# Optimization experiments

Measured on AMD Instinct MI355X. Metric: run time of the kernel, lower is better.

## Reference

```python
import jax, jax.numpy as jnp
import numpy as np

N = 100000   # total nodes
E = 600000   # total edges
G = 2048     # graphs in batch
DIN = 9      # input node feature dim
D = 128      # hidden == output dim
L = 5        # GIN layers
BN_EPS = 1e-5
LN_EPS = 1e-5


def setup_inputs() -> dict:
    key = jax.random.key(0)
    ks = jax.random.split(key, 24)
    s = 0.05
    x = jax.random.normal(ks[0], (N, DIN), jnp.float32)
    edge_index = jax.random.randint(ks[1], (2, E), 0, N, dtype=jnp.int32)
    batch = jnp.sort(jax.random.randint(ks[2], (N,), 0, G, dtype=jnp.int32))
    return {
        "x": x,
        "edge_index": edge_index,
        "batch": batch,
        # node embedding
        "node_emb_W": jax.random.normal(ks[3], (DIN, D), jnp.float32) * s,
        "node_emb_b": jnp.zeros((D,), jnp.float32),
        # GIN layer MLPs, stacked over layers: Linear(D,2D) -> ReLU -> Linear(2D,D)
        "W1s": jax.random.normal(ks[4], (L, D, 2 * D), jnp.float32) * s,
        "b1s": jnp.zeros((L, 2 * D), jnp.float32),
        "W2s": jax.random.normal(ks[5], (L, 2 * D, D), jnp.float32) * s,
        "b2s": jnp.zeros((L, D), jnp.float32),
        # BatchNorm affine params per layer
        "bn_g": jnp.ones((L, D), jnp.float32),
        "bn_b": jnp.zeros((L, D), jnp.float32),
        # virtual node
        "vn_emb": jax.random.normal(ks[6], (1, D), jnp.float32),
        "vn_W1": jax.random.normal(ks[7], (D, D), jnp.float32) * s,
        "vn_b1": jnp.zeros((D,), jnp.float32),
        "vn_W2": jax.random.normal(ks[8], (D, D), jnp.float32) * s,
        "vn_b2": jnp.zeros((D,), jnp.float32),
        # graph MLP: Linear -> LayerNorm -> ReLU -> Linear
        "gm_W1": jax.random.normal(ks[9], (D, D), jnp.float32) * s,
        "gm_b1": jnp.zeros((D,), jnp.float32),
        "ln_g": jnp.ones((D,), jnp.float32),
        "ln_b": jnp.zeros((D,), jnp.float32),
        "gm_W2": jax.random.normal(ks[10], (D, D), jnp.float32) * s,
        "gm_b2": jnp.zeros((D,), jnp.float32),
    }


def _mean_pool(h, batch):
    # segment mean over graphs: [N, D] -> [G, D]
    s = jax.ops.segment_sum(h, batch, num_segments=G)
    cnt = jax.ops.segment_sum(jnp.ones((h.shape[0], 1), h.dtype), batch, num_segments=G)
    return s / jnp.maximum(cnt, 1.0)


def _batchnorm(m, g, b):
    mu = jnp.mean(m, axis=0)
    var = jnp.mean(jnp.square(m - mu), axis=0)  # biased var (torch train-mode norm)
    return (m - mu) * jax.lax.rsqrt(var + BN_EPS) * g + b


def reference(x, edge_index, batch, node_emb_W, node_emb_b, W1s, b1s, W2s, b2s,
              bn_g, bn_b, vn_emb, vn_W1, vn_b1, vn_W2, vn_b2,
              gm_W1, gm_b1, ln_g, ln_b, gm_W2, gm_b2):
    src, dst = edge_index[0], edge_index[1]
    h = x @ node_emb_W + node_emb_b                       # [N, D]
    vn = jnp.tile(vn_emb, (G, 1))                         # [G, D]
    for i in range(L):
        h_prev = h
        # GINConv (eps=0): mlp(h + sum_{j->i} h_j) via gather/scatter-add
        agg = jax.ops.segment_sum(h[src], dst, num_segments=N)
        m = h + agg
        m = jax.nn.relu(m @ W1s[i] + b1s[i]) @ W2s[i] + b2s[i]
        h = jax.nn.relu(_batchnorm(m, bn_g[i], bn_b[i]))
        # (dropout is identity in eval mode)
        if i > 0:
            h = h + h_prev
        # virtual node: pool -> MLP -> broadcast back
        temp = _mean_pool(h, batch)                       # [G, D]
        vn = vn + (jax.nn.relu(temp @ vn_W1 + vn_b1) @ vn_W2 + vn_b2)
        h = h + vn[batch]
    node_features = h                                     # output_projection = Identity
    gf = _mean_pool(node_features, batch)                 # [G, D]
    gf = gf @ gm_W1 + gm_b1
    mu = jnp.mean(gf, axis=-1, keepdims=True)
    var = jnp.mean(jnp.square(gf - mu), axis=-1, keepdims=True)
    gf = (gf - mu) * jax.lax.rsqrt(var + LN_EPS) * ln_g + ln_b
    gf = jax.nn.relu(gf)
    graph_features = gf @ gm_W2 + gm_b2
    return node_features, graph_features
```

## Files before the change

kernel.cpp:

```cpp
#include <hip/hip_runtime.h>
#include <stdint.h>

#define NNODES 100000
#define NEDGES 600000
#define NGRAPH 2048
#define DD 128
#define NLAYER 5
#define NPAD 100096
#define SCAN_NB 391
#define NSTAT 32

typedef __attribute__((ext_vector_type(8))) __bf16 bf16x8;
typedef __attribute__((ext_vector_type(4))) float f32x4;
typedef __attribute__((ext_vector_type(8))) ushort u16x8;

__device__ __forceinline__ ushort f2b(float f) {
    union { float f; uint32_t u; } v; v.f = f;
    uint32_t r = v.u + 0x7FFFu + ((v.u >> 16) & 1u);
    return (ushort)(r >> 16);
}

__device__ __forceinline__ float b2f(ushort u) {
    union { uint32_t u; float f; } v; v.u = ((uint32_t)u) << 16; return v.f;
}

__device__ __forceinline__ void gload_lds16(const void* g, void* l) {
    __builtin_amdgcn_global_load_lds(
        (const __attribute__((address_space(1))) void*)g,
        (__attribute__((address_space(3))) void*)l, 16, 0, 0);
}

__global__ void prep_w_kernel(const float* __restrict__ W1s, const float* __restrict__ W2s,
                              ushort* __restrict__ w1t, ushort* __restrict__ w2t) {
    int idx = blockIdx.x * 256 + threadIdx.x;
    const int per = 128 * 256;
    if (idx < NLAYER * per) {
        int i = idx / per, rem = idx % per;
        int n = rem >> 7, k = rem & 127;
        w1t[idx] = f2b(W1s[(size_t)i * per + k * 256 + n]);
    } else if (idx < 2 * NLAYER * per) {
        int j = idx - NLAYER * per;
        int i = j / per, rem = j % per;
        int n = rem >> 8, k = rem & 255;
        w2t[j] = f2b(W2s[(size_t)i * per + k * 128 + n]);
    }
}

__global__ void node_embed_kernel(const float* __restrict__ x, const float* __restrict__ W,
                                  const float* __restrict__ b, ushort* __restrict__ hb,
                                  const float* __restrict__ vne, float* __restrict__ vn) {
    int idx = blockIdx.x * 256 + threadIdx.x;
    if (idx < NNODES * 128) {
        int n = idx >> 7, d = idx & 127;
        float v = b[d];
#pragma unroll
        for (int k = 0; k < 9; ++k) v += x[n * 9 + k] * W[k * 128 + d];
        hb[(size_t)n * 128 + d] = f2b(v);
    } else if (idx < NNODES * 128 + NGRAPH * 128) {
        int r = idx - NNODES * 128;
        vn[r] = vne[r & 127];
    }
}


__global__ void deg_kernel(const int* __restrict__ dst, int* __restrict__ deg) {
    int e = blockIdx.x * 256 + threadIdx.x;
    if (e < NEDGES) atomicAdd(&deg[dst[e]], 1);
}

__global__ void scan_part_kernel(const int* __restrict__ deg, int* __restrict__ partials) {
    int i = blockIdx.x * 256 + threadIdx.x;
    int lane = threadIdx.x & 63, w = threadIdx.x >> 6;
    int v = (i < NNODES) ? deg[i] : 0;
#pragma unroll
    for (int o = 1; o < 64; o <<= 1) v += __shfl_xor(v, o);
    __shared__ int ws[4];
    if (lane == 0) ws[w] = v;
    __syncthreads();
    if (threadIdx.x == 0) partials[blockIdx.x] = ws[0] + ws[1] + ws[2] + ws[3];
}

__global__ __launch_bounds__(512)
void scan_top_kernel(int* __restrict__ partials) {
    __shared__ int s[512];
    int t = threadIdx.x;
    int v = (t < SCAN_NB) ? partials[t] : 0;
    s[t] = v;
    __syncthreads();
#pragma unroll
    for (int o = 1; o < 512; o <<= 1) {
        int n = (t >= o) ? s[t - o] : 0;
        __syncthreads();
        s[t] += n;
        __syncthreads();
    }
    if (t < SCAN_NB) partials[t] = s[t] - v;
}

__global__ void scan_blocks_kernel(const int* __restrict__ deg, const int* __restrict__ partials,
                                   int* __restrict__ rs, int* __restrict__ cursor) {
    int i = blockIdx.x * 256 + threadIdx.x;
    int lane = threadIdx.x & 63, w = threadIdx.x >> 6;
    int v = (i < NNODES) ? deg[i] : 0;
    int x = v;
#pragma unroll
    for (int o = 1; o < 64; o <<= 1) {
        int n = __shfl_up(x, o);
        if (lane >= o) x += n;
    }
    __shared__ int ws[4];
    if (lane == 63) ws[w] = x;
    __syncthreads();
    if (threadIdx.x == 0) {
        int a = 0;
#pragma unroll
        for (int k = 0; k < 4; ++k) { int t = ws[k]; ws[k] = a; a += t; }
    }
    __syncthreads();
    int excl = (x - v) + ws[w] + partials[blockIdx.x];
    if (i < NNODES) { rs[i] = excl; cursor[i] = excl; }
    if (i == 0) rs[NNODES] = NEDGES;
}

__global__ void csr_scatter_kernel(const int* __restrict__ src, const int* __restrict__ dst,
                                   int* __restrict__ cursor, int* __restrict__ csrc) {
    int e = blockIdx.x * 256 + threadIdx.x;
    if (e < NEDGES) {
        int p = atomicAdd(&cursor[dst[e]], 1);
        csrc[p] = src[e];
    }
}

__device__ __forceinline__ int lbound(const int* __restrict__ b, int key) {
    int lo = 0, hi = NNODES;
    while (lo < hi) { int m = (lo + hi) >> 1; if (b[m] < key) lo = m + 1; else hi = m; }
    return lo;
}

__global__ void gstart_kernel(const int* __restrict__ batch, int* __restrict__ gstart,
                              float* __restrict__ inv) {
    int g = blockIdx.x * 256 + threadIdx.x;
    if (g <= NGRAPH)
        gstart[g] = (g == NGRAPH) ? NNODES : lbound(batch, g);
    if (g < NGRAPH) {
        int c = lbound(batch, g + 1) - lbound(batch, g);
        inv[g] = 1.f / (float)(c > 0 ? c : 1);
    }
}


__global__ __launch_bounds__(256)
void gin_agg_kernel(const ushort* __restrict__ hb, const int* __restrict__ rs,
                    const int* __restrict__ csrc, ushort* __restrict__ xb,
                    float* __restrict__ stats) {
    if (blockIdx.x < NSTAT) stats[blockIdx.x * 256 + threadIdx.x] = 0.f;
    int slot = threadIdx.x >> 4;
    int j = threadIdx.x & 15;
    int node = blockIdx.x * 16 + slot;
    if (node >= NNODES) return;
    int s = rs[node], e = rs[node + 1];
    u16x8 v0 = *(const u16x8*)(hb + (size_t)node * 128 + j * 8);
    float a[8], b[8];
#pragma unroll
    for (int t = 0; t < 8; ++t) { a[t] = b2f(v0[t]); b[t] = 0.f; }
    int k = s;
    for (; k + 3 < e; k += 4) {
        int s0 = csrc[k], s1 = csrc[k + 1], s2 = csrc[k + 2], s3 = csrc[k + 3];
        u16x8 va = *(const u16x8*)(hb + (size_t)s0 * 128 + j * 8);
        u16x8 vb = *(const u16x8*)(hb + (size_t)s1 * 128 + j * 8);
        u16x8 vc = *(const u16x8*)(hb + (size_t)s2 * 128 + j * 8);
        u16x8 vd = *(const u16x8*)(hb + (size_t)s3 * 128 + j * 8);
#pragma unroll
        for (int t = 0; t < 8; ++t) {
            a[t] += b2f(va[t]) + b2f(vc[t]);
            b[t] += b2f(vb[t]) + b2f(vd[t]);
        }
    }
    for (; k < e; ++k) {
        int s0 = csrc[k];
        u16x8 va = *(const u16x8*)(hb + (size_t)s0 * 128 + j * 8);
#pragma unroll
        for (int t = 0; t < 8; ++t) a[t] += b2f(va[t]);
    }
    u16x8 o;
#pragma unroll
    for (int t = 0; t < 8; ++t) o[t] = f2b(a[t] + b[t]);
    *(u16x8*)(xb + (size_t)node * 128 + j * 8) = o;
}

#define MLP_TILES 4
#define MLP_GRID 391
__global__ __launch_bounds__(256, 2)
void fused_mlp_kernel(const ushort* __restrict__ A, const ushort* __restrict__ W1,
                      const float* __restrict__ b1, const ushort* __restrict__ W2,
                      const float* __restrict__ b2, ushort* __restrict__ out_b,
                      float* __restrict__ stats) {
    __shared__ __align__(16) ushort lA[8192];
    __shared__ __align__(16) ushort mid[16384];
    const int tid = threadIdx.x;
    const int lane = tid & 63, w = tid >> 6;
    const int q = lane >> 4, l16 = lane & 15;
    float* sbase = stats + (blockIdx.x & (NSTAT - 1)) * 256;

    bf16x8 w1f[4][4], w2f[8][2];
#pragma unroll
    for (int ks = 0; ks < 4; ++ks)
#pragma unroll
        for (int ni = 0; ni < 4; ++ni)
            w1f[ks][ni] = *(const bf16x8*)(W1 + (size_t)(w * 64 + ni * 16 + l16) * 128 + ks * 32 + q * 8);
#pragma unroll
    for (int ks = 0; ks < 8; ++ks)
#pragma unroll
        for (int ni = 0; ni < 2; ++ni)
            w2f[ks][ni] = *(const bf16x8*)(W2 + (size_t)(w * 32 + ni * 16 + l16) * 256 + ks * 32 + q * 8);

    {
        int rb = blockIdx.x * (64 * MLP_TILES);
#pragma unroll
        for (int p = 0; p < 4; ++p)
            gload_lds16(A + (size_t)(rb + lane) * 128 + p * 32 + w * 8,
                        &lA[(size_t)(p * 256 + w * 64 + lane) * 8]);
    }

    for (int tt = 0; tt < MLP_TILES; ++tt) {
        const int rb = blockIdx.x * (64 * MLP_TILES) + tt * 64;
        __syncthreads();

        f32x4 acc1[4][4] = {};
#pragma unroll
        for (int ks = 0; ks < 4; ++ks) {
            bf16x8 af[4];
#pragma unroll
            for (int mi = 0; mi < 4; ++mi)
                af[mi] = *(const bf16x8*)&lA[ks * 2048 + q * 512 + (mi * 16 + l16) * 8];
#pragma unroll
            for (int mi = 0; mi < 4; ++mi)
#pragma unroll
                for (int ni = 0; ni < 4; ++ni)
                    acc1[mi][ni] = __builtin_amdgcn_mfma_f32_16x16x32_bf16(af[mi], w1f[ks][ni], acc1[mi][ni], 0, 0, 0);
        }

#pragma unroll
        for (int ni = 0; ni < 4; ++ni) {
            int col = w * 64 + ni * 16 + l16;
            float bs = b1[col];
            int g2 = col >> 3, jj = col & 7;
#pragma unroll
            for (int mi = 0; mi < 4; ++mi) {
                int rowb = mi * 16 + q * 4;
#pragma unroll
                for (int r = 0; r < 4; ++r) {
                    float v = acc1[mi][ni][r] + bs;
                    v = v > 0.f ? v : 0.f;
                    mid[g2 * 512 + (rowb + r) * 8 + jj] = f2b(v);
                }
            }
        }
        __syncthreads();

        if (tt + 1 < MLP_TILES) {
            int rb2 = rb + 64;
#pragma unroll
            for (int p = 0; p < 4; ++p)
                gload_lds16(A + (size_t)(rb2 + lane) * 128 + p * 32 + w * 8,
                            &lA[(size_t)(p * 256 + w * 64 + lane) * 8]);
        }

        f32x4 acc2[4][2] = {};
#pragma unroll
        for (int ks = 0; ks < 8; ++ks) {
            bf16x8 af[4];
#pragma unroll
            for (int mi = 0; mi < 4; ++mi)
                af[mi] = *(const bf16x8*)&mid[(ks * 4 + q) * 512 + (mi * 16 + l16) * 8];
#pragma unroll
            for (int mi = 0; mi < 4; ++mi)
#pragma unroll
                for (int ni = 0; ni < 2; ++ni)
                    acc2[mi][ni] = __builtin_amdgcn_mfma_f32_16x16x32_bf16(af[mi], w2f[ks][ni], acc2[mi][ni], 0, 0, 0);
        }

#pragma unroll
        for (int ni = 0; ni < 2; ++ni) {
            int col = w * 32 + ni * 16 + l16;
            float bs = b2[col];
            float s = 0.f, sq = 0.f;
#pragma unroll
            for (int mi = 0; mi < 4; ++mi) {
                int row = rb + mi * 16 + q * 4;
#pragma unroll
                for (int r = 0; r < 4; ++r) {
                    float v = acc2[mi][ni][r] + bs;
                    out_b[(size_t)(row + r) * 128 + col] = f2b(v);
                    if (row + r < NNODES) { s += v; sq += v * v; }
                }
            }
            s  += __shfl_xor(s, 16);  s  += __shfl_xor(s, 32);
            sq += __shfl_xor(sq, 16); sq += __shfl_xor(sq, 32);
            if (lane < 16) {
                atomicAdd(&sbase[col], s);
                atomicAdd(&sbase[128 + col], sq);
            }
        }
    }
}

__global__ __launch_bounds__(256)
void vn_update_kernel(const ushort* __restrict__ m, const ushort* __restrict__ hb,
                      const float* __restrict__ stats,
                      const float* __restrict__ bng, const float* __restrict__ bnb,
                      const int* __restrict__ gstart, const float* __restrict__ inv,
                      const float* __restrict__ W1, const float* __restrict__ b1,
                      const float* __restrict__ W2, const float* __restrict__ b2,
                      float* __restrict__ vn, int resid) {
    __shared__ float sC[128], sS[128];
    __shared__ float red[16][128];
    __shared__ float t[128], t1[128];
    int g = blockIdx.x, tid = threadIdx.x;
    if (tid < 128) {
        int d = tid;
        float sum = 0.f, sq = 0.f;
#pragma unroll
        for (int c = 0; c < NSTAT; ++c) {
            sum += stats[c * 256 + d];
            sq  += stats[c * 256 + 128 + d];
        }
        float mu = sum * (1.f / NNODES);
        float var = sq * (1.f / NNODES) - mu * mu;
        var = var < 0.f ? 0.f : var;
        float sc = bng[d] * rsqrtf(var + 1e-5f);
        sC[d] = sc;
        sS[d] = bnb[d] - mu * sc;
    }
    __syncthreads();
    int j = tid & 15, rg = tid >> 4;
    float sc8[8], sh8[8], acc[8];
#pragma unroll
    for (int k = 0; k < 8; ++k) { sc8[k] = sC[j * 8 + k]; sh8[k] = sS[j * 8 + k]; acc[k] = 0.f; }
    int s = gstart[g], e = gstart[g + 1];
    for (int r = s + rg; r < e; r += 16) {
        u16x8 mv = *(const u16x8*)(m + (size_t)r * 128 + j * 8);
        float v[8];
#pragma unroll
        for (int k = 0; k < 8; ++k) v[k] = fmaxf(b2f(mv[k]) * sc8[k] + sh8[k], 0.f);
        if (resid) {
            u16x8 hv = *(const u16x8*)(hb + (size_t)r * 128 + j * 8);
#pragma unroll
            for (int k = 0; k < 8; ++k) v[k] += b2f(hv[k]);
        }
#pragma unroll
        for (int k = 0; k < 8; ++k) acc[k] += v[k];
    }
#pragma unroll
    for (int k = 0; k < 8; ++k) red[rg][j * 8 + k] = acc[k];
    __syncthreads();
    if (tid < 128) {
        int d = tid;
        float tot = 0.f;
#pragma unroll
        for (int r2 = 0; r2 < 16; ++r2) tot += red[r2][d];
        t[d] = tot * inv[g];
    }
    __syncthreads();
    if (tid < 128) {
        int d = tid;
        float a = b1[d];
        for (int k = 0; k < 128; ++k) a += t[k] * W1[k * 128 + d];
        t1[d] = fmaxf(a, 0.f);
    }
    __syncthreads();
    if (tid < 128) {
        int d = tid;
        float o = b2[d];
        for (int k = 0; k < 128; ++k) o += t1[k] * W2[k * 128 + d];
        vn[g * 128 + d] += o;
    }
}

template<int FINAL>
__global__ __launch_bounds__(512)
void bn_vn_apply_kernel(const ushort* __restrict__ m, const float* __restrict__ stats,
                        const float* __restrict__ bng, const float* __restrict__ bnb,
                        const float* __restrict__ vn, const int* __restrict__ batch,
                        ushort* __restrict__ hb, float* __restrict__ outN, int resid) {
    __shared__ float sC[128], sS[128];
    if (threadIdx.x < 128) {
        int d = threadIdx.x;
        float sum = 0.f, sq = 0.f;
#pragma unroll
        for (int c = 0; c < NSTAT; ++c) {
            sum += stats[c * 256 + d];
            sq  += stats[c * 256 + 128 + d];
        }
        float mu = sum * (1.f / NNODES);
        float var = sq * (1.f / NNODES) - mu * mu;
        var = var < 0.f ? 0.f : var;
        float sc = bng[d] * rsqrtf(var + 1e-5f);
        sC[d] = sc;
        sS[d] = bnb[d] - mu * sc;
    }
    __syncthreads();
    int t = blockIdx.x * 512 + threadIdx.x;
    if (t >= NNODES * 16) return;
    int row = t >> 4, j = t & 15;
    int g = batch[row];
    float4 v0 = ((const float4*)(vn + (size_t)g * 128))[j * 2];
    float4 v1 = ((const float4*)(vn + (size_t)g * 128))[j * 2 + 1];
    float vg[8] = {v0.x, v0.y, v0.z, v0.w, v1.x, v1.y, v1.z, v1.w};
    u16x8 mu8 = *(const u16x8*)(m + (size_t)row * 128 + j * 8);
    float wv[8];
#pragma unroll
    for (int k = 0; k < 8; ++k)
        wv[k] = fmaxf(b2f(mu8[k]) * sC[j * 8 + k] + sS[j * 8 + k], 0.f) + vg[k];
    if (resid) {
        u16x8 hp = *(const u16x8*)(hb + (size_t)row * 128 + j * 8);
#pragma unroll
        for (int k = 0; k < 8; ++k) wv[k] += b2f(hp[k]);
    }
    u16x8 o;
#pragma unroll
    for (int k = 0; k < 8; ++k) o[k] = f2b(wv[k]);
    *(u16x8*)(hb + (size_t)row * 128 + j * 8) = o;
    if (FINAL) {
        float4* op = (float4*)(outN + (size_t)row * 128 + j * 8);
        op[0] = make_float4(wv[0], wv[1], wv[2], wv[3]);
        op[1] = make_float4(wv[4], wv[5], wv[6], wv[7]);
    }
}

__global__ __launch_bounds__(256)
void graph_mlp_kernel(const ushort* __restrict__ hb, const int* __restrict__ gstart,
                      const float* __restrict__ inv,
                      const float* __restrict__ W1, const float* __restrict__ b1,
                      const float* __restrict__ lng, const float* __restrict__ lnb,
                      const float* __restrict__ W2, const float* __restrict__ b2,
                      float* __restrict__ out) {
    __shared__ float red[16][128];
    __shared__ float t[128], t1[128], lred[2];
    int g = blockIdx.x, tid = threadIdx.x;
    int j = tid & 15, rg = tid >> 4;
    float acc[8];
#pragma unroll
    for (int k = 0; k < 8; ++k) acc[k] = 0.f;
    int s = gstart[g], e = gstart[g + 1];
    for (int r = s + rg; r < e; r += 16) {
        u16x8 hv = *(const u16x8*)(hb + (size_t)r * 128 + j * 8);
#pragma unroll
        for (int k = 0; k < 8; ++k) acc[k] += b2f(hv[k]);
    }
#pragma unroll
    for (int k = 0; k < 8; ++k) red[rg][j * 8 + k] = acc[k];
    __syncthreads();
    if (tid < 128) {
        int d = tid;
        float tot = 0.f;
#pragma unroll
        for (int r2 = 0; r2 < 16; ++r2) tot += red[r2][d];
        t[d] = tot * inv[g];
    }
    __syncthreads();
    float a = 0.f, dv = 0.f, varv = 0.f;
    if (tid < 128) {
        int d = tid;
        a = b1[d];
        for (int k = 0; k < 128; ++k) a += t[k] * W1[k * 128 + d];
        int lane = d & 63, w = d >> 6;
        float ssum = a;
#pragma unroll
        for (int o = 1; o < 64; o <<= 1) ssum += __shfl_xor(ssum, o);
        if (lane == 0) lred[w] = ssum;
    }
    __syncthreads();
    if (tid < 128) {
        int d = tid;
        int lane = d & 63, w = d >> 6;
        float mu = (lred[0] + lred[1]) * (1.f / 128.f);
        dv = a - mu;
        float qq = dv * dv;
#pragma unroll
        for (int o = 1; o < 64; o <<= 1) qq += __shfl_xor(qq, o);
        if (lane == 0) lred[w] = qq;
    }
    __syncthreads();
    if (tid < 128) {
        int d = tid;
        float var = (lred[0] + lred[1]) * (1.f / 128.f);
        float v = dv * rsqrtf(var + 1e-5f) * lng[d] + lnb[d];
        t1[d] = fmaxf(v, 0.f);
    }
    __syncthreads();
    if (tid < 128) {
        int d = tid;
        float o2 = b2[d];
        for (int k = 0; k < 128; ++k) o2 += t1[k] * W2[k * 128 + d];
        out[g * 128 + d] = o2;
    }
}

extern "C" void kernel_launch(void* const* d_in, const int* in_sizes, int n_in,
                              void* d_out, int out_size, void* d_ws, size_t ws_size,
                              hipStream_t stream) {
    const float* x    = (const float*)d_in[0];
    const int*   edge = (const int*)d_in[1];
    const int*   src  = edge;
    const int*   dst  = edge + NEDGES;
    const int*   batch = (const int*)d_in[2];
    const float* nW   = (const float*)d_in[3];
    const float* nb   = (const float*)d_in[4];
    const float* W1s  = (const float*)d_in[5];
    const float* b1s  = (const float*)d_in[6];
    const float* W2s  = (const float*)d_in[7];
    const float* b2s  = (const float*)d_in[8];
    const float* bng  = (const float*)d_in[9];
    const float* bnb  = (const float*)d_in[10];
    const float* vne  = (const float*)d_in[11];
    const float* vW1  = (const float*)d_in[12];
    const float* vb1  = (const float*)d_in[13];
    const float* vW2  = (const float*)d_in[14];
    const float* vb2  = (const float*)d_in[15];
    const float* gW1  = (const float*)d_in[16];
    const float* gb1  = (const float*)d_in[17];
    const float* lng  = (const float*)d_in[18];
    const float* lnb  = (const float*)d_in[19];
    const float* gW2  = (const float*)d_in[20];
    const float* gb2  = (const float*)d_in[21];

    char* ws = (char*)d_ws;
    auto alloc = [&](size_t bytes) { char* p = ws; ws += (bytes + 255) & ~(size_t)255; return p; };
    float*  stats = (float*)alloc((size_t)NSTAT * 256 * 4);
    ushort* hb    = (ushort*)alloc((size_t)NPAD * 128 * 2);
    ushort* mbuf  = (ushort*)alloc((size_t)NPAD * 128 * 2);
    ushort* xb    = (ushort*)alloc((size_t)NPAD * 128 * 2);
    float*  vn    = (float*)alloc((size_t)NGRAPH * 128 * 4);
    ushort* w1t   = (ushort*)alloc((size_t)NLAYER * 256 * 128 * 2);
    ushort* w2t   = (ushort*)alloc((size_t)NLAYER * 128 * 256 * 2);
    float*  inv   = (float*)alloc((size_t)NGRAPH * 4);
    int*    gstart= (int*)alloc((size_t)(NGRAPH + 1) * 4);
    int*    deg   = (int*)alloc((size_t)NNODES * 4);
    int*    rs    = (int*)alloc((size_t)(NNODES + 1) * 4);
    int*    cursor= (int*)alloc((size_t)NNODES * 4);
    int*    csrc  = (int*)alloc((size_t)NEDGES * 4);
    int*    partials = (int*)alloc((size_t)SCAN_NB * 4);

    float* outN = (float*)d_out;
    float* outG = outN + (size_t)NNODES * 128;

    hipMemsetAsync(stats, 0, (size_t)NSTAT * 256 * 4, stream);
    hipMemsetAsync(deg, 0, (size_t)NNODES * 4, stream);

    deg_kernel<<<(NEDGES + 255) / 256, 256, 0, stream>>>(dst, deg);
    scan_part_kernel<<<SCAN_NB, 256, 0, stream>>>(deg, partials);
    scan_top_kernel<<<1, 512, 0, stream>>>(partials);
    scan_blocks_kernel<<<SCAN_NB, 256, 0, stream>>>(deg, partials, rs, cursor);
    csr_scatter_kernel<<<(NEDGES + 255) / 256, 256, 0, stream>>>(src, dst, cursor, csrc);
    gstart_kernel<<<(NGRAPH + 256) / 256, 256, 0, stream>>>(batch, gstart, inv);

    prep_w_kernel<<<(2 * NLAYER * 128 * 256 + 255) / 256, 256, 0, stream>>>(W1s, W2s, w1t, w2t);
    node_embed_kernel<<<((NNODES + NGRAPH) * 128 + 255) / 256, 256, 0, stream>>>(
        x, nW, nb, hb, vne, vn);

    const int flatNB = (NNODES * 16 + 511) / 512;
    for (int i = 0; i < NLAYER; ++i) {
        gin_agg_kernel<<<(NNODES + 15) / 16, 256, 0, stream>>>(hb, rs, csrc, xb, stats);
        fused_mlp_kernel<<<MLP_GRID, 256, 0, stream>>>(
            xb, w1t + (size_t)i * 256 * 128, b1s + i * 256,
            w2t + (size_t)i * 128 * 256, b2s + i * 128, mbuf, stats);
        vn_update_kernel<<<NGRAPH, 256, 0, stream>>>(
            mbuf, hb, stats, bng + i * 128, bnb + i * 128, gstart, inv,
            vW1, vb1, vW2, vb2, vn, i > 0 ? 1 : 0);
        if (i < NLAYER - 1)
            bn_vn_apply_kernel<0><<<flatNB, 512, 0, stream>>>(
                mbuf, stats, bng + i * 128, bnb + i * 128, vn, batch, hb, nullptr, i > 0 ? 1 : 0);
        else
            bn_vn_apply_kernel<1><<<flatNB, 512, 0, stream>>>(
                mbuf, stats, bng + i * 128, bnb + i * 128, vn, batch, hb, outN, 1);
    }
    graph_mlp_kernel<<<NGRAPH, 256, 0, stream>>>(hb, gstart, inv, gW1, gb1, lng, lnb, gW2, gb2, outG);
}
```

Before: 613.5 us.

## Fuse virtual-node update and BN/VN apply into one per-graph tail kernel

```diff
diff --git a/kernel.cpp b/kernel.cpp
--- a/kernel.cpp
+++ b/kernel.cpp
@@ -9,6 +9,7 @@
 #define NPAD 100096
 #define SCAN_NB 391
 #define NSTAT 32
+#define MAXROWS 128
 
 typedef __attribute__((ext_vector_type(8))) __bf16 bf16x8;
 typedef __attribute__((ext_vector_type(4))) float f32x4;
@@ -305,17 +306,19 @@
     }
 }
 
+template<int FINAL>
 __global__ __launch_bounds__(256)
-void vn_update_kernel(const ushort* __restrict__ m, const ushort* __restrict__ hb,
-                      const float* __restrict__ stats,
-                      const float* __restrict__ bng, const float* __restrict__ bnb,
-                      const int* __restrict__ gstart, const float* __restrict__ inv,
-                      const float* __restrict__ W1, const float* __restrict__ b1,
-                      const float* __restrict__ W2, const float* __restrict__ b2,
-                      float* __restrict__ vn, int resid) {
+void tail_kernel(const ushort* __restrict__ m, ushort* __restrict__ hb,
+                 const float* __restrict__ stats,
+                 const float* __restrict__ bng, const float* __restrict__ bnb,
+                 const int* __restrict__ gstart, const float* __restrict__ inv,
+                 const float* __restrict__ W1, const float* __restrict__ b1,
+                 const float* __restrict__ W2, const float* __restrict__ b2,
+                 float* __restrict__ vn, float* __restrict__ outN, int resid) {
+    __shared__ __align__(16) ushort rowbuf[MAXROWS * 128];
     __shared__ float sC[128], sS[128];
     __shared__ float red[16][128];
-    __shared__ float t[128], t1[128];
+    __shared__ float t[128], t1[128], vns[128];
     int g = blockIdx.x, tid = threadIdx.x;
     if (tid < 128) {
         int d = tid;
@@ -338,6 +341,7 @@
 #pragma unroll
     for (int k = 0; k < 8; ++k) { sc8[k] = sC[j * 8 + k]; sh8[k] = sS[j * 8 + k]; acc[k] = 0.f; }
     int s = gstart[g], e = gstart[g + 1];
+
     for (int r = s + rg; r < e; r += 16) {
         u16x8 mv = *(const u16x8*)(m + (size_t)r * 128 + j * 8);
         float v[8];
@@ -350,6 +354,13 @@
         }
 #pragma unroll
         for (int k = 0; k < 8; ++k) acc[k] += v[k];
+        int idx = r - s;
+        if (idx < MAXROWS) {
+            u16x8 o;
+#pragma unroll
+            for (int k = 0; k < 8; ++k) o[k] = f2b(v[k]);
+            *(u16x8*)(rowbuf + idx * 128 + j * 8) = o;
+        }
     }
 #pragma unroll
     for (int k = 0; k < 8; ++k) red[rg][j * 8 + k] = acc[k];
@@ -373,58 +384,44 @@
         int d = tid;
         float o = b2[d];
         for (int k = 0; k < 128; ++k) o += t1[k] * W2[k * 128 + d];
-        vn[g * 128 + d] += o;
-    }
-}
-
-template<int FINAL>
-__global__ __launch_bounds__(512)
-void bn_vn_apply_kernel(const ushort* __restrict__ m, const float* __restrict__ stats,
-                        const float* __restrict__ bng, const float* __restrict__ bnb,
-                        const float* __restrict__ vn, const int* __restrict__ batch,
-                        ushort* __restrict__ hb, float* __restrict__ outN, int resid) {
-    __shared__ float sC[128], sS[128];
-    if (threadIdx.x < 128) {
-        int d = threadIdx.x;
-        float sum = 0.f, sq = 0.f;
-#pragma unroll
-        for (int c = 0; c < NSTAT; ++c) {
-            sum += stats[c * 256 + d];
-            sq  += stats[c * 256 + 128 + d];
-        }
-        float mu = sum * (1.f / NNODES);
-        float var = sq * (1.f / NNODES) - mu * mu;
-        var = var < 0.f ? 0.f : var;
-        float sc = bng[d] * rsqrtf(var + 1e-5f);
-        sC[d] = sc;
-        sS[d] = bnb[d] - mu * sc;
-    }
-    __syncthreads();
-    int t = blockIdx.x * 512 + threadIdx.x;
-    if (t >= NNODES * 16) return;
-    int row = t >> 4, j = t & 15;
-    int g = batch[row];
-    float4 v0 = ((const float4*)(vn + (size_t)g * 128))[j * 2];
-    float4 v1 = ((const float4*)(vn + (size_t)g * 128))[j * 2 + 1];
-    float vg[8] = {v0.x, v0.y, v0.z, v0.w, v1.x, v1.y, v1.z, v1.w};
-    u16x8 mu8 = *(const u16x8*)(m + (size_t)row * 128 + j * 8);
-    float wv[8];
-#pragma unroll
-    for (int k = 0; k < 8; ++k)
-        wv[k] = fmaxf(b2f(mu8[k]) * sC[j * 8 + k] + sS[j * 8 + k], 0.f) + vg[k];
-    if (resid) {
-        u16x8 hp = *(const u16x8*)(hb + (size_t)row * 128 + j * 8);
-#pragma unroll
-        for (int k = 0; k < 8; ++k) wv[k] += b2f(hp[k]);
-    }
-    u16x8 o;
-#pragma unroll
-    for (int k = 0; k < 8; ++k) o[k] = f2b(wv[k]);
-    *(u16x8*)(hb + (size_t)row * 128 + j * 8) = o;
-    if (FINAL) {
-        float4* op = (float4*)(outN + (size_t)row * 128 + j * 8);
-        op[0] = make_float4(wv[0], wv[1], wv[2], wv[3]);
-        op[1] = make_float4(wv[4], wv[5], wv[6], wv[7]);
+        float vnew = vn[(size_t)g * 128 + d] + o;
+        vn[(size_t)g * 128 + d] = vnew;
+        vns[d] = vnew;
+    }
+    __syncthreads();
+
+    float vg[8];
+#pragma unroll
+    for (int k = 0; k < 8; ++k) vg[k] = vns[j * 8 + k];
+
+    for (int r = s + rg; r < e; r += 16) {
+        int idx = r - s;
+        float v[8];
+        if (idx < MAXROWS) {
+            u16x8 wv = *(const u16x8*)(rowbuf + idx * 128 + j * 8);
+#pragma unroll
+            for (int k = 0; k < 8; ++k) v[k] = b2f(wv[k]);
+        } else {
+            u16x8 mv = *(const u16x8*)(m + (size_t)r * 128 + j * 8);
+#pragma unroll
+            for (int k = 0; k < 8; ++k) v[k] = fmaxf(b2f(mv[k]) * sc8[k] + sh8[k], 0.f);
+            if (resid) {
+                u16x8 hv = *(const u16x8*)(hb + (size_t)r * 128 + j * 8);
+#pragma unroll
+                for (int k = 0; k < 8; ++k) v[k] += b2f(hv[k]);
+            }
+        }
+#pragma unroll
+        for (int k = 0; k < 8; ++k) v[k] += vg[k];
+        u16x8 o;
+#pragma unroll
+        for (int k = 0; k < 8; ++k) o[k] = f2b(v[k]);
+        *(u16x8*)(hb + (size_t)r * 128 + j * 8) = o;
+        if (FINAL) {
+            float4* op = (float4*)(outN + (size_t)r * 128 + j * 8);
+            op[0] = make_float4(v[0], v[1], v[2], v[3]);
+            op[1] = make_float4(v[4], v[5], v[6], v[7]);
+        }
     }
 }
 
@@ -459,7 +456,7 @@
         t[d] = tot * inv[g];
     }
     __syncthreads();
-    float a = 0.f, dv = 0.f, varv = 0.f;
+    float a = 0.f, dv = 0.f;
     if (tid < 128) {
         int d = tid;
         a = b1[d];
@@ -559,21 +556,19 @@
     node_embed_kernel<<<((NNODES + NGRAPH) * 128 + 255) / 256, 256, 0, stream>>>(
         x, nW, nb, hb, vne, vn);
 
-    const int flatNB = (NNODES * 16 + 511) / 512;
     for (int i = 0; i < NLAYER; ++i) {
         gin_agg_kernel<<<(NNODES + 15) / 16, 256, 0, stream>>>(hb, rs, csrc, xb, stats);
         fused_mlp_kernel<<<MLP_GRID, 256, 0, stream>>>(
             xb, w1t + (size_t)i * 256 * 128, b1s + i * 256,
             w2t + (size_t)i * 128 * 256, b2s + i * 128, mbuf, stats);
-        vn_update_kernel<<<NGRAPH, 256, 0, stream>>>(
-            mbuf, hb, stats, bng + i * 128, bnb + i * 128, gstart, inv,
-            vW1, vb1, vW2, vb2, vn, i > 0 ? 1 : 0);
         if (i < NLAYER - 1)
-            bn_vn_apply_kernel<0><<<flatNB, 512, 0, stream>>>(
-                mbuf, stats, bng + i * 128, bnb + i * 128, vn, batch, hb, nullptr, i > 0 ? 1 : 0);
+            tail_kernel<0><<<NGRAPH, 256, 0, stream>>>(
+                mbuf, hb, stats, bng + i * 128, bnb + i * 128, gstart, inv,
+                vW1, vb1, vW2, vb2, vn, nullptr, i > 0 ? 1 : 0);
         else
-            bn_vn_apply_kernel<1><<<flatNB, 512, 0, stream>>>(
-                mbuf, stats, bng + i * 128, bnb + i * 128, vn, batch, hb, outN, 1);
+            tail_kernel<1><<<NGRAPH, 256, 0, stream>>>(
+                mbuf, hb, stats, bng + i * 128, bnb + i * 128, gstart, inv,
+                vW1, vb1, vW2, vb2, vn, outN, 1);
     }
     graph_mlp_kernel<<<NGRAPH, 256, 0, stream>>>(hb, gstart, inv, gW1, gb1, lng, lnb, gW2, gb2, outG);
 }
```

New measurement: 595.7 us. 2.9% less time.
